# Kernel tuning notes

Measured on AMD Instinct MI355X. Metric: run time of the kernel, lower is better.

Reference implementation:

```python
import jax, jax.numpy as jnp
import numpy as np

HORIZON = 8


def _gru_pass(seq, h0, w_ih, w_hh, b_ih, b_hh):
    """Run a single-layer PyTorch-convention GRU over seq (batch_first) starting
    from hidden h0; return the final hidden state (== out[:, -1, :]).
    seq: [B, T, I], h0: [B, H], w_ih: [3H, I], w_hh: [3H, H].
    Gate order (PyTorch): r, z, n."""
    # Precompute input projections for all timesteps: [B, T, 3H] -> [T, B, 3H]
    x_proj = jnp.einsum('bti,gi->btg', seq, w_ih) + b_ih
    x_proj = jnp.swapaxes(x_proj, 0, 1)

    def step(h, xp):
        hp = h @ w_hh.T + b_hh                      # [B, 3H]
        xr, xz, xn = jnp.split(xp, 3, axis=-1)
        hr, hz, hn = jnp.split(hp, 3, axis=-1)
        r = jax.nn.sigmoid(xr + hr)
        z = jax.nn.sigmoid(xz + hz)
        n = jnp.tanh(xn + r * hn)
        h_new = (1.0 - z) * n + z * h
        return h_new, None

    h_final, _ = jax.lax.scan(step, h0, x_proj)
    return h_final


def setup_inputs() -> dict:
    key = jax.random.key(0)
    ks = jax.random.split(key, 7)
    B, T, I, H = 256, 256, 64, 512
    scale = 0.04  # ~1/sqrt(H), matches PyTorch uniform init magnitude
    return {
        'x': jax.random.normal(ks[0], (B, T, I), dtype=jnp.float32),
        'w_ih': jax.random.normal(ks[1], (3 * H, I), dtype=jnp.float32) * scale,
        'w_hh': jax.random.normal(ks[2], (3 * H, H), dtype=jnp.float32) * scale,
        'b_ih': jax.random.normal(ks[3], (3 * H,), dtype=jnp.float32) * scale,
        'b_hh': jax.random.normal(ks[4], (3 * H,), dtype=jnp.float32) * scale,
        'fc_w': jax.random.normal(ks[5], (I, H), dtype=jnp.float32) * scale,
        'fc_b': jax.random.normal(ks[6], (I,), dtype=jnp.float32) * scale,
    }


def reference(x, w_ih, w_hh, b_ih, b_hh, fc_w, fc_b):
    """Faithful translation of PredictorRNN.forward: each horizon step re-runs
    the GRU over the whole growing sequence, carrying hidden state h between
    passes (matching the original torch code's out,h = rnn(seq, h))."""
    B = x.shape[0]
    H = w_hh.shape[1]
    h = jnp.zeros((B, H), dtype=x.dtype)  # h=None -> zeros in torch
    seq = x
    preds = []
    for _ in range(HORIZON):
        h = _gru_pass(seq, h, w_ih, w_hh, b_ih, b_hh)  # == out[:, -1, :]
        step = h @ fc_w.T + fc_b                       # [B, I]
        preds.append(step)
        seq = jnp.concatenate([seq, step[:, None, :]], axis=1)
    return jnp.stack(preds, axis=1)  # [B, horizon, I]
```

## Files before the change

kernel.cpp:

```cpp
#include <hip/hip_runtime.h>


typedef __attribute__((ext_vector_type(8))) short short8;
typedef __attribute__((ext_vector_type(4))) float floatx4;

#define B_    256
#define T_    256
#define I_    64
#define H_    512
#define HZ    8
#define LPAD  520
#define HLSZ  (16 * LPAD)

#define MFMA_BF16(acc, a, b) \
  acc = __builtin_amdgcn_mfma_f32_16x16x32_bf16((a), (b), (acc), 0, 0, 0)

#define POLL_BACKOFF(it)                         \
  do {                                           \
    if ((it) < 2)      __builtin_amdgcn_s_sleep(1);  \
    else if ((it) < 8) __builtin_amdgcn_s_sleep(4);  \
    else               __builtin_amdgcn_s_sleep(16); \
  } while (0)

__device__ __forceinline__ float bf2f(unsigned short u) {
  union { unsigned int i; float f; } v; v.i = ((unsigned int)u) << 16; return v.f;
}
__device__ __forceinline__ unsigned short f2bf(float f) {
  union { float f; unsigned int i; } v; v.f = f;
  return (unsigned short)((v.i + 0x7FFFu + ((v.i >> 16) & 1u)) >> 16);
}
__device__ __forceinline__ short8 ld8_f32_to_bf16(const float* p) {
  short8 r;
#pragma unroll
  for (int e = 0; e < 8; ++e) r[e] = (short)f2bf(p[e]);
  return r;
}
__device__ __forceinline__ float sigm(float xx) {
  return __builtin_amdgcn_rcpf(1.f + __expf(-xx));
}
__device__ __forceinline__ float tanh_fast(float xx) {
  float e = __expf(2.f * xx);
  return 1.f - 2.f * __builtin_amdgcn_rcpf(e + 1.f);
}
__device__ __forceinline__ unsigned long long ald64(const unsigned int* p) {
  return __hip_atomic_load((const unsigned long long*)p, __ATOMIC_RELAXED,
                           __HIP_MEMORY_SCOPE_AGENT);
}
__device__ __forceinline__ void ast32(unsigned int* p, unsigned int v) {
  __hip_atomic_store(p, v, __ATOMIC_RELAXED, __HIP_MEMORY_SCOPE_AGENT);
}

__device__ __forceinline__ void stage_h16(unsigned short* hl,
                                          const unsigned int* hb,
                                          unsigned int want, int tid,
                                          int& dly) {
  for (int i = 0; i < dly; ++i) __builtin_amdgcn_s_sleep(2);
  unsigned long long v[16];
#pragma unroll
  for (int i = 0; i < 16; ++i)
    v[i] = ald64(hb + (size_t)i * H_ + 2 * tid);
  bool fail1 = false;
  int it = 0;
  for (;;) {
    bool all = true;
#pragma unroll
    for (int i = 0; i < 16; ++i) {
      unsigned int w0 = (unsigned int)v[i];
      unsigned int w1 = (unsigned int)(v[i] >> 32);
      if (((w0 >> 16) != want) || ((w1 >> 16) != want)) all = false;
    }
    if (all) break;
    if (it == 0) fail1 = true;
    __builtin_amdgcn_s_sleep(2);
#pragma unroll
    for (int i = 0; i < 16; ++i) {
      unsigned int w0 = (unsigned int)v[i];
      unsigned int w1 = (unsigned int)(v[i] >> 32);
      if (((w0 >> 16) != want) || ((w1 >> 16) != want))
        v[i] = ald64(hb + (size_t)i * H_ + 2 * tid);
    }
    ++it;
  }
  if (__any((int)fail1)) { if (dly < 12) dly += 2; }
  else                   { if (dly > 0)  dly -= 1; }
#pragma unroll
  for (int i = 0; i < 16; ++i) {
    unsigned int w0 = (unsigned int)v[i];
    unsigned int w1 = (unsigned int)(v[i] >> 32);
    *(unsigned int*)&hl[i * LPAD + 2 * tid] = (w0 & 0xffffu) | (w1 << 16);
  }
}

extern "C" __global__ void __launch_bounds__(256, 1)
gru_chain(const float* __restrict__ x,
          const float* __restrict__ w_ih,
          const float* __restrict__ w_hh,
          const float* __restrict__ b_ih,
          const float* __restrict__ b_hh,
          const float* __restrict__ fc_w,
          const float* __restrict__ fc_b,
          float* __restrict__ out,
          unsigned int* __restrict__ hbuf,
          unsigned int* __restrict__ xext)
{
  const int tid  = threadIdx.x;
  const int wave = tid >> 6;
  const int lane = tid & 63;
  const int bx   = blockIdx.x;
  const int grp  = bx & 15;
  const int ju   = ((bx >> 4) << 2) | wave;
  const int n16  = lane & 15;
  const int quad = lane >> 4;
  const int jg   = ju * 16 + n16;
  const int rowbase = grp * 16;

  __shared__ __align__(16) unsigned short hls[2 * HLSZ];

  short8 wR[18], wZ[18], wHN[16], wXN[2];
  {
    const int koff = quad * 8;
    const float* whr = w_hh + (size_t)(0 * H_ + jg) * H_ + koff;
    const float* whz = w_hh + (size_t)(1 * H_ + jg) * H_ + koff;
    const float* whn = w_hh + (size_t)(2 * H_ + jg) * H_ + koff;
#pragma unroll
    for (int kc = 0; kc < 16; ++kc) {
      wR[kc]  = ld8_f32_to_bf16(whr + kc * 32);
      wZ[kc]  = ld8_f32_to_bf16(whz + kc * 32);
      wHN[kc] = ld8_f32_to_bf16(whn + kc * 32);
    }
    const float* wir = w_ih + (size_t)(0 * H_ + jg) * I_ + koff;
    const float* wiz = w_ih + (size_t)(1 * H_ + jg) * I_ + koff;
    const float* win = w_ih + (size_t)(2 * H_ + jg) * I_ + koff;
#pragma unroll
    for (int kc = 0; kc < 2; ++kc) {
      wR[16 + kc] = ld8_f32_to_bf16(wir + kc * 32);
      wZ[16 + kc] = ld8_f32_to_bf16(wiz + kc * 32);
      wXN[kc]     = ld8_f32_to_bf16(win + kc * 32);
    }
  }
  const float brc = b_ih[jg]          + b_hh[jg];
  const float bzc = b_ih[H_ + jg]     + b_hh[H_ + jg];
  const float bxn = b_ih[2 * H_ + jg];
  const float bhn = b_hh[2 * H_ + jg];

  float hloc[4] = {0.f, 0.f, 0.f, 0.f};
  int   dly = 4;

  int s = 0;
  for (int p = 0; p < HZ; ++p) {
    const int Tp = T_ + p;
    for (int t = 0; t < Tp; ++t) {
      short8 xaf0, xaf1;
      if (t < T_) {
        const float* xs = x + ((size_t)(rowbase + n16) * T_ + t) * I_ + quad * 8;
        xaf0 = ld8_f32_to_bf16(xs);
        xaf1 = ld8_f32_to_bf16(xs + 32);
      }
      unsigned short* hl = &hls[(s & 1) * HLSZ];
      if (s > 0) {
        const unsigned int* hb = hbuf + (size_t)((s + 1) & 1) * (B_ * H_) +
                                 (size_t)rowbase * H_;
        stage_h16(hl, hb, (unsigned int)s, tid, dly);
      } else {
#pragma unroll
        for (int i = 0; i < 16; ++i)
          *(unsigned int*)&hl[i * LPAD + 2 * tid] = 0u;
      }
      if (t >= T_) {
        const int p2 = t - T_;
        const unsigned int wantx = (unsigned int)(p2 + 1);
        const unsigned int* xb =
            xext + ((size_t)p2 * B_ + rowbase + n16) * I_;
        unsigned long long u[8];
#pragma unroll
        for (int k = 0; k < 8; ++k) {
          int off = (k < 4) ? (quad * 8 + 2 * k) : (32 + quad * 8 + 2 * (k - 4));
          u[k] = ald64(xb + off);
        }
        int it = 0;
        for (;;) {
          bool all = true;
#pragma unroll
          for (int k = 0; k < 8; ++k) {
            unsigned int w0 = (unsigned int)u[k];
            unsigned int w1 = (unsigned int)(u[k] >> 32);
            if (((w0 >> 16) != wantx) || ((w1 >> 16) != wantx)) {
              all = false;
              int off = (k < 4) ? (quad * 8 + 2 * k)
                                : (32 + quad * 8 + 2 * (k - 4));
              u[k] = ald64(xb + off);
            }
          }
          if (all) break;
          POLL_BACKOFF(it);
          ++it;
        }
#pragma unroll
        for (int k = 0; k < 4; ++k) {
          xaf0[2 * k]     = (short)(unsigned short)u[k];
          xaf0[2 * k + 1] = (short)(unsigned short)(u[k] >> 32);
          xaf1[2 * k]     = (short)(unsigned short)u[4 + k];
          xaf1[2 * k + 1] = (short)(unsigned short)(u[4 + k] >> 32);
        }
      }
      __syncthreads();
      short8 haf[16];
#pragma unroll
      for (int kc = 0; kc < 16; ++kc)
        haf[kc] = *(const short8*)&hl[n16 * LPAD + kc * 32 + quad * 8];

      floatx4 aR = {0.f, 0.f, 0.f, 0.f};
      floatx4 aZ = {0.f, 0.f, 0.f, 0.f};
      floatx4 aN = {0.f, 0.f, 0.f, 0.f};
      floatx4 aX = {0.f, 0.f, 0.f, 0.f};
#pragma unroll
      for (int kc = 0; kc < 16; ++kc) {
        MFMA_BF16(aR, haf[kc], wR[kc]);
        MFMA_BF16(aZ, haf[kc], wZ[kc]);
        MFMA_BF16(aN, haf[kc], wHN[kc]);
      }
      MFMA_BF16(aR, xaf0, wR[16]);  MFMA_BF16(aR, xaf1, wR[17]);
      MFMA_BF16(aZ, xaf0, wZ[16]);  MFMA_BF16(aZ, xaf1, wZ[17]);
      MFMA_BF16(aX, xaf0, wXN[0]);  MFMA_BF16(aX, xaf1, wXN[1]);

      unsigned int* hd = hbuf + (size_t)(s & 1) * (B_ * H_);
      const unsigned int tg = ((unsigned int)(s + 1)) << 16;
      unsigned int hv[4];
#pragma unroll
      for (int i = 0; i < 4; ++i) {
        float rv = sigm(aR[i] + brc);
        float zv = sigm(aZ[i] + bzc);
        float nv = tanh_fast(aX[i] + bxn + rv * (aN[i] + bhn));
        float hn = (1.f - zv) * nv + zv * hloc[i];
        hloc[i]  = hn;
        hv[i]    = tg | (unsigned int)f2bf(hn);
      }
#pragma unroll
      for (int i = 0; i < 4; ++i)
        ast32(&hd[(size_t)(rowbase + quad * 4 + i) * H_ + jg], hv[i]);
      ++s;
    }
    {
      unsigned short* hl = &hls[(s & 1) * HLSZ];
      const unsigned int* hb = hbuf + (size_t)((s + 1) & 1) * (B_ * H_) +
                               (size_t)rowbase * H_;
      stage_h16(hl, hb, (unsigned int)s, tid, dly);
      __syncthreads();
      const int mm  = lane & 15;
      const int sub = lane >> 4;
#pragma unroll
      for (int cc = 0; cc < 2; ++cc) {
        const int c = ju * 2 + cc;
        const unsigned short* hrow = &hl[mm * LPAD + sub * 128];
        const float* wrow = fc_w + (size_t)c * H_ + sub * 128;
        float acc = 0.f;
#pragma unroll
        for (int kk = 0; kk < 128; kk += 8) {
          short8 hv2 = *(const short8*)(hrow + kk);
#pragma unroll
          for (int e = 0; e < 8; ++e)
            acc = fmaf(bf2f((unsigned short)hv2[e]), wrow[kk + e], acc);
        }
        acc += __shfl_xor(acc, 16, 64);
        acc += __shfl_xor(acc, 32, 64);
        if (sub == 0) {
          float val = acc + fc_b[c];
          out[((size_t)(rowbase + mm) * HZ + p) * I_ + c] = val;
          ast32(&xext[((size_t)p * B_ + rowbase + mm) * I_ + c],
                (((unsigned int)(p + 1)) << 16) | (unsigned int)f2bf(val));
        }
      }
      __syncthreads();
    }
  }
}

extern "C" void kernel_launch(void* const* d_in, const int* in_sizes, int n_in,
                              void* d_out, int out_size, void* d_ws, size_t ws_size,
                              hipStream_t stream) {
  const float* x    = (const float*)d_in[0];
  const float* w_ih = (const float*)d_in[1];
  const float* w_hh = (const float*)d_in[2];
  const float* b_ih = (const float*)d_in[3];
  const float* b_hh = (const float*)d_in[4];
  const float* fc_w = (const float*)d_in[5];
  const float* fc_b = (const float*)d_in[6];
  float* out = (float*)d_out;

  unsigned char* ws = (unsigned char*)d_ws;
  const size_t hbuf_b = (size_t)2 * B_ * H_ * 4;
  const size_t xext_b = (size_t)HZ * B_ * I_ * 4;
  unsigned int* hbuf = (unsigned int*)ws;
  unsigned int* xext = (unsigned int*)(ws + hbuf_b);

  hipMemsetAsync(d_ws, 0, hbuf_b + xext_b, stream);

  gru_chain<<<dim3(128), dim3(256), 0, stream>>>(
      x, w_ih, w_hh, b_ih, b_hh, fc_w, fc_b, out, hbuf, xext);
}
```

Baseline: 6.178 ms.

## Interleave two row groups per block to overlap hidden-state polling with compute

```diff
diff --git a/kernel.cpp b/kernel.cpp
--- a/kernel.cpp
+++ b/kernel.cpp
@@ -50,46 +50,151 @@
   __hip_atomic_store(p, v, __ATOMIC_RELAXED, __HIP_MEMORY_SCOPE_AGENT);
 }
 
-__device__ __forceinline__ void stage_h16(unsigned short* hl,
-                                          const unsigned int* hb,
-                                          unsigned int want, int tid,
-                                          int& dly) {
-  for (int i = 0; i < dly; ++i) __builtin_amdgcn_s_sleep(2);
-  unsigned long long v[16];
-#pragma unroll
-  for (int i = 0; i < 16; ++i)
-    v[i] = ald64(hb + (size_t)i * H_ + 2 * tid);
-  bool fail1 = false;
-  int it = 0;
-  for (;;) {
-    bool all = true;
-#pragma unroll
-    for (int i = 0; i < 16; ++i) {
-      unsigned int w0 = (unsigned int)v[i];
-      unsigned int w1 = (unsigned int)(v[i] >> 32);
-      if (((w0 >> 16) != want) || ((w1 >> 16) != want)) all = false;
-    }
-    if (all) break;
-    if (it == 0) fail1 = true;
-    __builtin_amdgcn_s_sleep(2);
-#pragma unroll
-    for (int i = 0; i < 16; ++i) {
-      unsigned int w0 = (unsigned int)v[i];
-      unsigned int w1 = (unsigned int)(v[i] >> 32);
-      if (((w0 >> 16) != want) || ((w1 >> 16) != want))
-        v[i] = ald64(hb + (size_t)i * H_ + 2 * tid);
-    }
-    ++it;
-  }
-  if (__any((int)fail1)) { if (dly < 12) dly += 2; }
-  else                   { if (dly > 0)  dly -= 1; }
-#pragma unroll
-  for (int i = 0; i < 16; ++i) {
-    unsigned int w0 = (unsigned int)v[i];
-    unsigned int w1 = (unsigned int)(v[i] >> 32);
-    *(unsigned int*)&hl[i * LPAD + 2 * tid] = (w0 & 0xffffu) | (w1 << 16);
-  }
-}
+#define ISSUE_SWEEP(v, rowb, par)                                          \
+  do {                                                                     \
+    const unsigned int* hbp_ = hbuf + (size_t)(par) * (B_ * H_) +          \
+                               (size_t)(rowb) * H_;                        \
+    _Pragma("unroll") for (int i_ = 0; i_ < 16; ++i_)                      \
+        v[i_] = ald64(hbp_ + (size_t)i_ * H_ + 2 * tid);                   \
+  } while (0)
+
+#define VERIFY_STAGE(v, rowb, par, want_, hl)                              \
+  do {                                                                     \
+    const unsigned int* hbp_ = hbuf + (size_t)(par) * (B_ * H_) +          \
+                               (size_t)(rowb) * H_;                        \
+    const unsigned int want__ = (unsigned int)(want_);                     \
+    for (;;) {                                                             \
+      bool all_ = true;                                                    \
+      _Pragma("unroll") for (int i_ = 0; i_ < 16; ++i_) {                  \
+        unsigned int w0_ = (unsigned int)v[i_];                            \
+        unsigned int w1_ = (unsigned int)(v[i_] >> 32);                    \
+        if (((w0_ >> 16) != want__) || ((w1_ >> 16) != want__))            \
+          all_ = false;                                                    \
+      }                                                                    \
+      if (all_) break;                                                     \
+      __builtin_amdgcn_s_sleep(2);                                         \
+      _Pragma("unroll") for (int i_ = 0; i_ < 16; ++i_) {                  \
+        unsigned int w0_ = (unsigned int)v[i_];                            \
+        unsigned int w1_ = (unsigned int)(v[i_] >> 32);                    \
+        if (((w0_ >> 16) != want__) || ((w1_ >> 16) != want__))            \
+          v[i_] = ald64(hbp_ + (size_t)i_ * H_ + 2 * tid);                 \
+      }                                                                    \
+    }                                                                      \
+    _Pragma("unroll") for (int i_ = 0; i_ < 16; ++i_) {                    \
+      unsigned int w0_ = (unsigned int)v[i_];                              \
+      unsigned int w1_ = (unsigned int)(v[i_] >> 32);                      \
+      *(unsigned int*)&hl[i_ * LPAD + 2 * tid] =                           \
+          (w0_ & 0xffffu) | (w1_ << 16);                                   \
+    }                                                                      \
+  } while (0)
+
+#define HALF_STEP(RC, HLC, HLOC, VC, RO, VO, IP, DOISSUE)                  \
+  do {                                                                     \
+    short8 xaf0, xaf1;                                                     \
+    if (t < T_) {                                                          \
+      const float* xs_ =                                                   \
+          x + ((size_t)((RC) + n16) * T_ + t) * I_ + quad * 8;             \
+      xaf0 = ld8_f32_to_bf16(xs_);                                         \
+      xaf1 = ld8_f32_to_bf16(xs_ + 32);                                    \
+    }                                                                      \
+    unsigned short* hl = (HLC) + (s & 1) * HLSZ;                           \
+    if (s > 0) {                                                           \
+      VERIFY_STAGE(VC, RC, (s + 1) & 1, s, hl);                            \
+    } else {                                                               \
+      _Pragma("unroll") for (int i_ = 0; i_ < 16; ++i_)                    \
+          *(unsigned int*)&hl[i_ * LPAD + 2 * tid] = 0u;                   \
+    }                                                                      \
+    if (t >= T_) {                                                         \
+      const int p2_ = t - T_;                                              \
+      const unsigned int wx_ = (unsigned int)(p2_ + 1);                    \
+      const unsigned int* xb_ =                                            \
+          xext + ((size_t)p2_ * B_ + (RC) + n16) * I_;                     \
+      unsigned long long u_[8];                                            \
+      _Pragma("unroll") for (int k_ = 0; k_ < 8; ++k_) {                   \
+        int off_ = (k_ < 4) ? (quad * 8 + 2 * k_)                          \
+                            : (32 + quad * 8 + 2 * (k_ - 4));              \
+        u_[k_] = ald64(xb_ + off_);                                        \
+      }                                                                    \
+      int it_ = 0;                                                         \
+      for (;;) {                                                           \
+        bool all_ = true;                                                  \
+        _Pragma("unroll") for (int k_ = 0; k_ < 8; ++k_) {                 \
+          unsigned int w0_ = (unsigned int)u_[k_];                         \
+          unsigned int w1_ = (unsigned int)(u_[k_] >> 32);                 \
+          if (((w0_ >> 16) != wx_) || ((w1_ >> 16) != wx_)) {              \
+            all_ = false;                                                  \
+            int off_ = (k_ < 4) ? (quad * 8 + 2 * k_)                      \
+                                : (32 + quad * 8 + 2 * (k_ - 4));          \
+            u_[k_] = ald64(xb_ + off_);                                    \
+          }                                                                \
+        }                                                                  \
+        if (all_) break;                                                   \
+        POLL_BACKOFF(it_);                                                 \
+        ++it_;                                                             \
+      }                                                                    \
+      _Pragma("unroll") for (int k_ = 0; k_ < 4; ++k_) {                   \
+        xaf0[2 * k_]     = (short)(unsigned short)u_[k_];                  \
+        xaf0[2 * k_ + 1] = (short)(unsigned short)(u_[k_] >> 32);          \
+        xaf1[2 * k_]     = (short)(unsigned short)u_[4 + k_];              \
+        xaf1[2 * k_ + 1] = (short)(unsigned short)(u_[4 + k_] >> 32);      \
+      }                                                                    \
+    }                                                                      \
+    __syncthreads();                                                       \
+    if (DOISSUE) ISSUE_SWEEP(VO, RO, IP);                                  \
+    short8 haf[16];                                                        \
+    _Pragma("unroll") for (int kc = 0; kc < 16; ++kc)                      \
+        haf[kc] = *(const short8*)&hl[n16 * LPAD + kc * 32 + quad * 8];    \
+    floatx4 aR = {0.f, 0.f, 0.f, 0.f};                                     \
+    floatx4 aZ = {0.f, 0.f, 0.f, 0.f};                                     \
+    floatx4 aN = {0.f, 0.f, 0.f, 0.f};                                     \
+    floatx4 aX = {0.f, 0.f, 0.f, 0.f};                                     \
+    _Pragma("unroll") for (int kc = 0; kc < 16; ++kc) {                    \
+      MFMA_BF16(aR, haf[kc], wR[kc]);                                      \
+      MFMA_BF16(aZ, haf[kc], wZ[kc]);                                      \
+      MFMA_BF16(aN, haf[kc], wHN[kc]);                                     \
+    }                                                                      \
+    MFMA_BF16(aR, xaf0, wR[16]);  MFMA_BF16(aR, xaf1, wR[17]);             \
+    MFMA_BF16(aZ, xaf0, wZ[16]);  MFMA_BF16(aZ, xaf1, wZ[17]);             \
+    MFMA_BF16(aX, xaf0, wXN[0]);  MFMA_BF16(aX, xaf1, wXN[1]);             \
+    unsigned int* hd_ = hbuf + (size_t)(s & 1) * (B_ * H_);                \
+    const unsigned int tg_ = ((unsigned int)(s + 1)) << 16;                \
+    unsigned int hv_[4];                                                   \
+    _Pragma("unroll") for (int i_ = 0; i_ < 4; ++i_) {                     \
+      float rv = sigm(aR[i_] + brc);                                       \
+      float zv = sigm(aZ[i_] + bzc);                                       \
+      float nv = tanh_fast(aX[i_] + bxn + rv * (aN[i_] + bhn));            \
+      float hn = (1.f - zv) * nv + zv * (HLOC)[i_];                        \
+      (HLOC)[i_] = hn;                                                     \
+      hv_[i_]    = tg_ | (unsigned int)f2bf(hn);                           \
+    }                                                                      \
+    _Pragma("unroll") for (int i_ = 0; i_ < 4; ++i_)                       \
+        ast32(&hd_[(size_t)((RC) + quad * 4 + i_) * H_ + jg], hv_[i_]);    \
+  } while (0)
+
+#define FC_CHAIN(RC, hl)                                                   \
+  do {                                                                     \
+    const int mm  = lane & 15;                                             \
+    const int sub = lane >> 4;                                             \
+    _Pragma("unroll") for (int cc = 0; cc < 2; ++cc) {                     \
+      const int c = ju * 2 + cc;                                           \
+      const unsigned short* hrow = &hl[mm * LPAD + sub * 128];             \
+      const float* wrow = fc_w + (size_t)c * H_ + sub * 128;               \
+      float acc = 0.f;                                                     \
+      _Pragma("unroll") for (int kk = 0; kk < 128; kk += 8) {              \
+        short8 hv2 = *(const short8*)(hrow + kk);                          \
+        _Pragma("unroll") for (int e = 0; e < 8; ++e)                      \
+            acc = fmaf(bf2f((unsigned short)hv2[e]), wrow[kk + e], acc);   \
+      }                                                                    \
+      acc += __shfl_xor(acc, 16, 64);                                      \
+      acc += __shfl_xor(acc, 32, 64);                                      \
+      if (sub == 0) {                                                      \
+        float val = acc + fc_b[c];                                         \
+        out[((size_t)((RC) + mm) * HZ + p) * I_ + c] = val;                \
+        ast32(&xext[((size_t)p * B_ + (RC) + mm) * I_ + c],                \
+              (((unsigned int)(p + 1)) << 16) | (unsigned int)f2bf(val));  \
+      }                                                                    \
+    }                                                                      \
+  } while (0)
 
 extern "C" __global__ void __launch_bounds__(256, 1)
 gru_chain(const float* __restrict__ x,
@@ -107,14 +212,18 @@
   const int wave = tid >> 6;
   const int lane = tid & 63;
   const int bx   = blockIdx.x;
-  const int grp  = bx & 15;
-  const int ju   = ((bx >> 4) << 2) | wave;
+  const int q    = bx & 7;
+  const int cblk = bx >> 3;
+  const int ju   = (cblk << 2) | wave;
   const int n16  = lane & 15;
   const int quad = lane >> 4;
   const int jg   = ju * 16 + n16;
-  const int rowbase = grp * 16;
-
-  __shared__ __align__(16) unsigned short hls[2 * HLSZ];
+  const int rA   = q * 16;
+  const int rB   = (q + 8) * 16;
+
+  __shared__ __align__(16) unsigned short hls[4 * HLSZ];
+  unsigned short* hlsA = hls;
+  unsigned short* hlsB = hls + 2 * HLSZ;
 
   short8 wR[18], wZ[18], wHN[16], wXN[2];
   {
@@ -143,134 +252,30 @@
   const float bxn = b_ih[2 * H_ + jg];
   const float bhn = b_hh[2 * H_ + jg];
 
-  float hloc[4] = {0.f, 0.f, 0.f, 0.f};
-  int   dly = 4;
+  float hlocA[4] = {0.f, 0.f, 0.f, 0.f};
+  float hlocB[4] = {0.f, 0.f, 0.f, 0.f};
+  unsigned long long vA[16], vB[16];
 
   int s = 0;
   for (int p = 0; p < HZ; ++p) {
     const int Tp = T_ + p;
     for (int t = 0; t < Tp; ++t) {
-      short8 xaf0, xaf1;
-      if (t < T_) {
-        const float* xs = x + ((size_t)(rowbase + n16) * T_ + t) * I_ + quad * 8;
-        xaf0 = ld8_f32_to_bf16(xs);
-        xaf1 = ld8_f32_to_bf16(xs + 32);
-      }
-      unsigned short* hl = &hls[(s & 1) * HLSZ];
-      if (s > 0) {
-        const unsigned int* hb = hbuf + (size_t)((s + 1) & 1) * (B_ * H_) +
-                                 (size_t)rowbase * H_;
-        stage_h16(hl, hb, (unsigned int)s, tid, dly);
-      } else {
-#pragma unroll
-        for (int i = 0; i < 16; ++i)
-          *(unsigned int*)&hl[i * LPAD + 2 * tid] = 0u;
-      }
-      if (t >= T_) {
-        const int p2 = t - T_;
-        const unsigned int wantx = (unsigned int)(p2 + 1);
-        const unsigned int* xb =
-            xext + ((size_t)p2 * B_ + rowbase + n16) * I_;
-        unsigned long long u[8];
-#pragma unroll
-        for (int k = 0; k < 8; ++k) {
-          int off = (k < 4) ? (quad * 8 + 2 * k) : (32 + quad * 8 + 2 * (k - 4));
-          u[k] = ald64(xb + off);
-        }
-        int it = 0;
-        for (;;) {
-          bool all = true;
-#pragma unroll
-          for (int k = 0; k < 8; ++k) {
-            unsigned int w0 = (unsigned int)u[k];
-            unsigned int w1 = (unsigned int)(u[k] >> 32);
-            if (((w0 >> 16) != wantx) || ((w1 >> 16) != wantx)) {
-              all = false;
-              int off = (k < 4) ? (quad * 8 + 2 * k)
-                                : (32 + quad * 8 + 2 * (k - 4));
-              u[k] = ald64(xb + off);
-            }
-          }
-          if (all) break;
-          POLL_BACKOFF(it);
-          ++it;
-        }
-#pragma unroll
-        for (int k = 0; k < 4; ++k) {
-          xaf0[2 * k]     = (short)(unsigned short)u[k];
-          xaf0[2 * k + 1] = (short)(unsigned short)(u[k] >> 32);
-          xaf1[2 * k]     = (short)(unsigned short)u[4 + k];
-          xaf1[2 * k + 1] = (short)(unsigned short)(u[4 + k] >> 32);
-        }
-      }
-      __syncthreads();
-      short8 haf[16];
-#pragma unroll
-      for (int kc = 0; kc < 16; ++kc)
-        haf[kc] = *(const short8*)&hl[n16 * LPAD + kc * 32 + quad * 8];
-
-      floatx4 aR = {0.f, 0.f, 0.f, 0.f};
-      floatx4 aZ = {0.f, 0.f, 0.f, 0.f};
-      floatx4 aN = {0.f, 0.f, 0.f, 0.f};
-      floatx4 aX = {0.f, 0.f, 0.f, 0.f};
-#pragma unroll
-      for (int kc = 0; kc < 16; ++kc) {
-        MFMA_BF16(aR, haf[kc], wR[kc]);
-        MFMA_BF16(aZ, haf[kc], wZ[kc]);
-        MFMA_BF16(aN, haf[kc], wHN[kc]);
-      }
-      MFMA_BF16(aR, xaf0, wR[16]);  MFMA_BF16(aR, xaf1, wR[17]);
-      MFMA_BF16(aZ, xaf0, wZ[16]);  MFMA_BF16(aZ, xaf1, wZ[17]);
-      MFMA_BF16(aX, xaf0, wXN[0]);  MFMA_BF16(aX, xaf1, wXN[1]);
-
-      unsigned int* hd = hbuf + (size_t)(s & 1) * (B_ * H_);
-      const unsigned int tg = ((unsigned int)(s + 1)) << 16;
-      unsigned int hv[4];
-#pragma unroll
-      for (int i = 0; i < 4; ++i) {
-        float rv = sigm(aR[i] + brc);
-        float zv = sigm(aZ[i] + bzc);
-        float nv = tanh_fast(aX[i] + bxn + rv * (aN[i] + bhn));
-        float hn = (1.f - zv) * nv + zv * hloc[i];
-        hloc[i]  = hn;
-        hv[i]    = tg | (unsigned int)f2bf(hn);
-      }
-#pragma unroll
-      for (int i = 0; i < 4; ++i)
-        ast32(&hd[(size_t)(rowbase + quad * 4 + i) * H_ + jg], hv[i]);
+      HALF_STEP(rA, hlsA, hlocA, vA, rB, vB, (s + 1) & 1, s >= 1);
+      HALF_STEP(rB, hlsB, hlocB, vB, rA, vA, s & 1, 1);
       ++s;
     }
     {
-      unsigned short* hl = &hls[(s & 1) * HLSZ];
-      const unsigned int* hb = hbuf + (size_t)((s + 1) & 1) * (B_ * H_) +
-                               (size_t)rowbase * H_;
-      stage_h16(hl, hb, (unsigned int)s, tid, dly);
+      ISSUE_SWEEP(vB, rB, (s + 1) & 1);
+      unsigned short* hlA = hlsA + (s & 1) * HLSZ;
+      VERIFY_STAGE(vA, rA, (s + 1) & 1, s, hlA);
       __syncthreads();
-      const int mm  = lane & 15;
-      const int sub = lane >> 4;
-#pragma unroll
-      for (int cc = 0; cc < 2; ++cc) {
-        const int c = ju * 2 + cc;
-        const unsigned short* hrow = &hl[mm * LPAD + sub * 128];
-        const float* wrow = fc_w + (size_t)c * H_ + sub * 128;
-        float acc = 0.f;
-#pragma unroll
-        for (int kk = 0; kk < 128; kk += 8) {
-          short8 hv2 = *(const short8*)(hrow + kk);
-#pragma unroll
-          for (int e = 0; e < 8; ++e)
-            acc = fmaf(bf2f((unsigned short)hv2[e]), wrow[kk + e], acc);
-        }
-        acc += __shfl_xor(acc, 16, 64);
-        acc += __shfl_xor(acc, 32, 64);
-        if (sub == 0) {
-          float val = acc + fc_b[c];
-          out[((size_t)(rowbase + mm) * HZ + p) * I_ + c] = val;
-          ast32(&xext[((size_t)p * B_ + rowbase + mm) * I_ + c],
-                (((unsigned int)(p + 1)) << 16) | (unsigned int)f2bf(val));
-        }
-      }
+      FC_CHAIN(rA, hlA);
+      unsigned short* hlB = hlsB + (s & 1) * HLSZ;
+      VERIFY_STAGE(vB, rB, (s + 1) & 1, s, hlB);
       __syncthreads();
+      FC_CHAIN(rB, hlB);
+      __syncthreads();
+      if (p + 1 < HZ) ISSUE_SWEEP(vA, rA, (s + 1) & 1);
     }
   }
 }
@@ -295,6 +300,6 @@
 
   hipMemsetAsync(d_ws, 0, hbuf_b + xext_b, stream);
 
-  gru_chain<<<dim3(128), dim3(256), 0, stream>>>(
+  gru_chain<<<dim3(64), dim3(256), 0, stream>>>(
       x, w_ih, w_hh, b_ih, b_hh, fc_w, fc_b, out, hbuf, xext);
 }
```

Result: slower. 12.22 ms (+97.8%).
